# Kernel tuning notes

Hardware: AMD Instinct MI355X
Metric: run time of the kernel (lower is better)

The kernel has to match this reference:

```python
import jax, jax.numpy as jnp
import numpy as np

EPS = 1e-12
K_APPNP = 3
ALPHA = 0.5

def setup_inputs() -> dict:
    key = jax.random.key(0)
    kg, kz, k1, k2, k3 = jax.random.split(key, 5)
    N, out_dim, hid_dim = 10000, 128, 256
    g = jax.random.uniform(kg, (N, N), dtype=jnp.float32)
    z = jax.random.normal(kz, (N, out_dim), dtype=jnp.float32)
    def xavier(k, shape):
        fan_out, fan_in = shape
        lim = float(np.sqrt(6.0 / (fan_in + fan_out)))
        return jax.random.uniform(k, shape, jnp.float32, -lim, lim)
    # torch Linear weight is [out_features, in_features]
    W1 = xavier(k1, (hid_dim, out_dim))    # res1: out_dim -> hid_dim
    W1_ = xavier(k2, (hid_dim, hid_dim))   # res1_: hid -> hid
    W2 = xavier(k3, (out_dim, hid_dim))    # res2: hid -> out_dim
    return {"g": g, "z": z, "W1": W1, "W1_": W1_, "W2": W2}

def _graph_conv(g, x, W, act):
    # dropout is identity in eval mode
    return act((g @ x) @ W.T)

def _appnp(g, H):
    Z = H
    for _ in range(K_APPNP):
        Z = (1.0 - ALPHA) * (g @ Z) + ALPHA * H
    return Z

def reference(g, z, W1, W1_, W2):
    z1 = _graph_conv(g, z, W1, jax.nn.relu)       # [N, hid]
    z_ = _graph_conv(g, z1, W1_, jax.nn.relu)     # [N, hid]
    # torch.tensor(z_) detaches from the autograd graph
    zn = jax.lax.stop_gradient(z_)
    norm = jnp.maximum(jnp.linalg.norm(zn, axis=1, keepdims=True), EPS)
    zn = zn / norm                                 # F.normalize(p=2, dim=1)
    Z = _appnp(g, zn)                              # [N, hid]
    res = _graph_conv(g, z_, W2, jax.nn.sigmoid)   # [N, out]
    return (res, Z)
```

## Files before the change

kernel.cpp:

```cpp
#include <hip/hip_runtime.h>
#include <stdint.h>

typedef __attribute__((ext_vector_type(8))) short short8;
typedef __attribute__((ext_vector_type(4))) float f32x4;
typedef __attribute__((ext_vector_type(4))) unsigned short us4;

#define MFMA16(a,b,c) __builtin_amdgcn_mfma_f32_16x16x32_bf16((a),(b),(c),0,0,0)

static __device__ __forceinline__ float bf2f(unsigned short u){
  union { float f; unsigned int i; } c; c.i = ((unsigned int)u) << 16; return c.f;
}
static __device__ __forceinline__ unsigned short f2bf(float f){
  union { float f; unsigned int i; } c; c.f = f;
  unsigned int x = c.i;
  unsigned int r = x + 0x7fffu + ((x >> 16) & 1u);
  return (unsigned short)(r >> 16);
}

typedef const __attribute__((address_space(1))) void cg_void;
typedef __attribute__((address_space(3))) void lds_void;
static __device__ __forceinline__ void gl_lds16(const void* g, void* l){
  __builtin_amdgcn_global_load_lds((cg_void*)g, (lds_void*)l, 16, 0, 0);
}

#define MROWS 10240LL

__global__ void k_conv_g(const float* __restrict__ g, unsigned short* __restrict__ o){
  const int CH = 2512;
  const long long total = 10240LL * CH;
  for (long long i = (long long)blockIdx.x*blockDim.x + threadIdx.x; i < total;
       i += (long long)gridDim.x*blockDim.x){
    int r = (int)(i / CH);
    int c4 = (int)(i % CH) * 4;
    us4 v = {0,0,0,0};
    if (r < 10000 && c4 < 10000){
      float4 f = *(const float4*)(g + (long long)r*10000 + c4);
      v.x = f2bf(f.x); v.y = f2bf(f.y); v.z = f2bf(f.z); v.w = f2bf(f.w);
    }
    *(us4*)(o + (long long)r*10048 + c4) = v;
  }
}

__global__ void k_conv_w(const float* __restrict__ a, unsigned short* __restrict__ oa, int na4,
                         const float* __restrict__ b, unsigned short* __restrict__ ob, int nb4,
                         const float* __restrict__ c, unsigned short* __restrict__ oc, int nc4){
  for (int i = blockIdx.x*blockDim.x + threadIdx.x; i < na4 + nb4 + nc4;
       i += gridDim.x*blockDim.x){
    const float* src; unsigned short* dst; int j = i;
    if (j < na4){ src = a; dst = oa; }
    else if (j < na4 + nb4){ j -= na4; src = b; dst = ob; }
    else { j -= na4 + nb4; src = c; dst = oc; }
    float4 f = *(const float4*)(src + (long long)j*4);
    us4 v; v.x=f2bf(f.x); v.y=f2bf(f.y); v.z=f2bf(f.z); v.w=f2bf(f.w);
    *(us4*)(dst + (long long)j*4) = v;
  }
}

__global__ void k_tconv_z(const float* __restrict__ z, unsigned short* __restrict__ o){
  __shared__ unsigned short t[64][65];
  const int rb = blockIdx.x*64, cb = blockIdx.y*64;
  #pragma unroll
  for (int it = 0; it < 4; ++it){
    int idx = it*256 + threadIdx.x;
    int r = idx >> 4, c4 = (idx & 15) * 4;
    float4 f = {0.f,0.f,0.f,0.f};
    if (rb + r < 10000) f = *(const float4*)(z + (long long)(rb+r)*128 + cb + c4);
    t[c4+0][r] = f2bf(f.x); t[c4+1][r] = f2bf(f.y);
    t[c4+2][r] = f2bf(f.z); t[c4+3][r] = f2bf(f.w);
  }
  __syncthreads();
  #pragma unroll
  for (int it = 0; it < 4; ++it){
    int idx = it*256 + threadIdx.x;
    int ro = idx >> 4, co4 = (idx & 15) * 4;
    us4 v; v.x=t[ro][co4]; v.y=t[ro][co4+1]; v.z=t[ro][co4+2]; v.w=t[ro][co4+3];
    *(us4*)(o + (long long)(cb+ro)*10048 + rb + co4) = v;
  }
}

__global__ void k_t_bf16(const unsigned short* __restrict__ in, unsigned short* __restrict__ o){
  __shared__ unsigned short t[64][65];
  const int rb = blockIdx.x*64, cb = blockIdx.y*64;
  #pragma unroll
  for (int it = 0; it < 4; ++it){
    int idx = it*256 + threadIdx.x;
    int r = idx >> 4, c4 = (idx & 15) * 4;
    us4 v = {0,0,0,0};
    if (rb + r < 10000) v = *(const us4*)(in + (long long)(rb+r)*256 + cb + c4);
    t[c4+0][r]=v.x; t[c4+1][r]=v.y; t[c4+2][r]=v.z; t[c4+3][r]=v.w;
  }
  __syncthreads();
  #pragma unroll
  for (int it = 0; it < 4; ++it){
    int idx = it*256 + threadIdx.x;
    int ro = idx >> 4, co4 = (idx & 15)*4;
    us4 v; v.x=t[ro][co4]; v.y=t[ro][co4+1]; v.z=t[ro][co4+2]; v.w=t[ro][co4+3];
    *(us4*)(o + (long long)(cb+ro)*10048 + rb + co4) = v;
  }
}

__global__ __launch_bounds__(512)
void k_gemm8(const unsigned short* __restrict__ A,
             const unsigned short* __restrict__ B,
             float* __restrict__ P, int S, int ldp)
{
  constexpr int LDA = 10048;
  __shared__ unsigned short sm[2][32768];

  const int tid = threadIdx.x;
  const int wid = tid >> 6, l = tid & 63;
  const int wm = wid >> 2, wn = wid & 3;
  const int lr = l & 15, lk = l >> 4;
  const int mBase = blockIdx.x * 256;
  const int nBase = blockIdx.y * 256;
  const int s = blockIdx.z;
  const int kt0 = (157 * s) / S, kt1 = (157 * (s + 1)) / S;

  const unsigned short* gsrc[8];
  int ldst[8];
  #pragma unroll
  for (int h = 0; h < 4; ++h){
    const unsigned short* base = (h < 2) ? A : B;
    const int rowBase = ((h < 2) ? mBase : nBase) + (h & 1) * 128;
    const int ldsOff = ((h < 2) ? 0 : 16384) + (h & 1) * 8192;
    #pragma unroll
    for (int i = 0; i < 2; ++i){
      int ch = tid + 512 * i;
      int row = ch >> 3, gc = (ch & 7) ^ (row & 7);
      gsrc[h*2+i] = base + (long long)(rowBase + row) * LDA + gc * 8;
      ldst[h*2+i] = ldsOff + ch * 8;
    }
  }
  auto stage_tile = [&](unsigned short* dst, int kt){
    const long long ko = (long long)kt * 64;
    #pragma unroll
    for (int i = 0; i < 8; ++i)
      gl_lds16(gsrc[i] + ko, dst + ldst[i]);
  };

  f32x4 acc[8][4];
  #pragma unroll
  for (int i = 0; i < 8; ++i)
    #pragma unroll
    for (int j = 0; j < 4; ++j){ f32x4 zz = {0.f,0.f,0.f,0.f}; acc[i][j] = zz; }

  stage_tile(&sm[0][0], kt0);

  int cur = 0;
  for (int kt = kt0; kt < kt1; ++kt){
    const bool pf = (kt + 1 < kt1);
    unsigned short* nb = &sm[cur ^ 1][0];
    const unsigned short* sp = &sm[cur][0];

    if (pf){
      stage_tile(nb, kt + 1);
      __builtin_amdgcn_sched_barrier(0);
      asm volatile("s_waitcnt vmcnt(8)" ::: "memory");
    } else {
      asm volatile("s_waitcnt vmcnt(0)" ::: "memory");
    }
    __builtin_amdgcn_sched_barrier(0);
    __builtin_amdgcn_s_barrier();
    __builtin_amdgcn_sched_barrier(0);

    short8 bfr[4][2];
    #pragma unroll
    for (int jj = 0; jj < 4; ++jj){
      const int row = wn*64 + jj*16 + lr;
      #pragma unroll
      for (int ks = 0; ks < 2; ++ks)
        bfr[jj][ks] = *(const short8*)(sp + 16384 + row*64 + (((ks*4 + lk) ^ (row & 7)) * 8));
    }
    #pragma unroll
    for (int ih = 0; ih < 2; ++ih){
      short8 af[4][2];
      #pragma unroll
      for (int ii = 0; ii < 4; ++ii){
        const int row = wm*128 + ih*64 + ii*16 + lr;
        #pragma unroll
        for (int ks = 0; ks < 2; ++ks)
          af[ii][ks] = *(const short8*)(sp + row*64 + (((ks*4 + lk) ^ (row & 7)) * 8));
      }
      __builtin_amdgcn_s_setprio(1);
      #pragma unroll
      for (int ks = 0; ks < 2; ++ks)
        #pragma unroll
        for (int ii = 0; ii < 4; ++ii)
          #pragma unroll
          for (int jj = 0; jj < 4; ++jj)
            acc[ih*4+ii][jj] = MFMA16(af[ii][ks], bfr[jj][ks], acc[ih*4+ii][jj]);
      __builtin_amdgcn_s_setprio(0);
    }
    __builtin_amdgcn_sched_barrier(0);
    __builtin_amdgcn_s_barrier();
    __builtin_amdgcn_sched_barrier(0);
    cur ^= 1;
  }

  float* Pp = P + (long long)s * MROWS * ldp;
  #pragma unroll
  for (int i = 0; i < 8; ++i){
    const int row0 = mBase + wm*128 + i*16 + lk*4;
    #pragma unroll
    for (int j = 0; j < 4; ++j){
      const int col = nBase + wn*64 + j*16 + lr;
      #pragma unroll
      for (int r = 0; r < 4; ++r)
        Pp[(long long)(row0 + r)*ldp + col] = acc[i][j][r];
    }
  }
}

template<int BN, int NWM, int NWN>
__global__ __launch_bounds__(256)
void k_gemm(const unsigned short* __restrict__ A,
            const unsigned short* __restrict__ B,
            float* __restrict__ P, int S, int ldp)
{
  constexpr int LDA = 10048;
  constexpr int BM  = 64;
  constexpr int WM = BM / NWM, WN = BN / NWN;
  constexpr int MF = WM / 16, NF = WN / 16;
  constexpr int AE = BM * 64;
  constexpr int BE = BN * 64;
  constexpr int ACH = BM * 8 / 256;
  constexpr int BCH = BN * 8 / 256;

  __shared__ unsigned short sm[2][AE + BE];

  const int tid = threadIdx.x, w = tid >> 6, l = tid & 63;
  const int lr = l & 15, lk = l >> 4, swz = l & 7;
  const int wm = w / NWN, wn = w % NWN;
  const int mBase = blockIdx.x * BM;
  const int nBase = blockIdx.y * BN;
  const int s = blockIdx.z;
  const int kt0 = (157 * s) / S, kt1 = (157 * (s + 1)) / S;

  auto stage = [&](int buf, int kt){
    unsigned short* dst = &sm[buf][0];
    const unsigned short* Ak = A + (long long)kt * 64;
    const unsigned short* Bk = B + (long long)kt * 64;
    #pragma unroll
    for (int i = 0; i < ACH; ++i){
      int c = i * 256 + tid;
      int row = c >> 3, gr = c & 7;
      gl_lds16(Ak + (long long)(mBase + row) * LDA + ((gr ^ (row & 7)) * 8),
               dst + c * 8);
    }
    #pragma unroll
    for (int i = 0; i < BCH; ++i){
      int c = i * 256 + tid;
      int row = c >> 3, gr = c & 7;
      gl_lds16(Bk + (long long)(nBase + row) * LDA + ((gr ^ (row & 7)) * 8),
               dst + AE + c * 8);
    }
  };

  f32x4 acc[MF][NF];
  #pragma unroll
  for (int i = 0; i < MF; ++i)
    #pragma unroll
    for (int j = 0; j < NF; ++j){ f32x4 zz = {0.f,0.f,0.f,0.f}; acc[i][j] = zz; }

  stage(0, kt0);
  int cur = 0;
  for (int kt = kt0; kt < kt1; ++kt){
    __syncthreads();
    if (kt + 1 < kt1) stage(cur ^ 1, kt + 1);
    const unsigned short* sp = &sm[cur][0];
    #pragma unroll
    for (int ks = 0; ks < 2; ++ks){
      short8 a[MF], b[NF];
      #pragma unroll
      for (int i = 0; i < MF; ++i){
        int row = wm * WM + i * 16 + lr;
        a[i] = *(const short8*)(sp + row * 64 + (((4*ks + lk) ^ swz) * 8));
      }
      #pragma unroll
      for (int j = 0; j < NF; ++j){
        int row = wn * WN + j * 16 + lr;
        b[j] = *(const short8*)(sp + AE + row * 64 + (((4*ks + lk) ^ swz) * 8));
      }
      #pragma unroll
      for (int i = 0; i < MF; ++i)
        #pragma unroll
        for (int j = 0; j < NF; ++j)
          acc[i][j] = MFMA16(a[i], b[j], acc[i][j]);
    }
    cur ^= 1;
  }

  float* Pp = P + (long long)s * MROWS * ldp;
  #pragma unroll
  for (int i = 0; i < MF; ++i){
    const int row0 = mBase + wm * WM + i * 16 + lk * 4;
    #pragma unroll
    for (int j = 0; j < NF; ++j){
      const int col = nBase + wn * WN + j * 16 + lr;
      #pragma unroll
      for (int r = 0; r < 4; ++r)
        Pp[(long long)(row0 + r) * ldp + col] = acc[i][j][r];
    }
  }
}

template<int EPI>
__global__ void k_reduce(const float* __restrict__ P, int S, int ldp, int colOff,
                         int lg, void* __restrict__ out, int ldc,
                         const unsigned short* __restrict__ H)
{
  const long long stride = MROWS * ldp;
  const int idx = blockIdx.x * 256 + threadIdx.x;
  const int row = idx >> lg;
  const int c4 = (idx & ((1 << lg) - 1)) * 4;
  const float* p = P + (long long)row * ldp + colOff + c4;
  float4 sv = *(const float4*)p;
  for (int s2 = 1; s2 < S; ++s2){
    float4 t = *(const float4*)(p + (long long)s2 * stride);
    sv.x += t.x; sv.y += t.y; sv.z += t.z; sv.w += t.w;
  }
  if constexpr (EPI == 2){
    us4 h = *(const us4*)(H + (long long)row * 256 + c4);
    sv.x = 0.5f*sv.x + 0.5f*bf2f(h.x);
    sv.y = 0.5f*sv.y + 0.5f*bf2f(h.y);
    sv.z = 0.5f*sv.z + 0.5f*bf2f(h.z);
    sv.w = 0.5f*sv.w + 0.5f*bf2f(h.w);
    *(float4*)((float*)out + (long long)row * ldc + c4) = sv;
  } else {
    us4 o; o.x=f2bf(sv.x); o.y=f2bf(sv.y); o.z=f2bf(sv.z); o.w=f2bf(sv.w);
    *(us4*)((unsigned short*)out + (long long)row * ldc + c4) = o;
  }
}

__global__ void k_reduce_T(const float* __restrict__ P, int S, int ldp, int colOff,
                           unsigned short* __restrict__ outT,
                           const unsigned short* __restrict__ H)
{
  __shared__ unsigned short t[64][65];
  const int rb = blockIdx.x*64, cb = blockIdx.y*64;
  const long long stride = MROWS * (long long)ldp;
  #pragma unroll
  for (int it = 0; it < 4; ++it){
    int idx = it*256 + threadIdx.x;
    int r = idx >> 4, c4 = (idx & 15)*4;
    int row = rb + r;
    float4 sv = {0.f,0.f,0.f,0.f};
    if (row < 10000){
      const float* p = P + (long long)row*ldp + colOff + cb + c4;
      sv = *(const float4*)p;
      for (int s2 = 1; s2 < S; ++s2){
        float4 tt = *(const float4*)(p + (long long)s2*stride);
        sv.x += tt.x; sv.y += tt.y; sv.z += tt.z; sv.w += tt.w;
      }
      us4 h = *(const us4*)(H + (long long)row*256 + cb + c4);
      sv.x = 0.5f*sv.x + 0.5f*bf2f(h.x);
      sv.y = 0.5f*sv.y + 0.5f*bf2f(h.y);
      sv.z = 0.5f*sv.z + 0.5f*bf2f(h.z);
      sv.w = 0.5f*sv.w + 0.5f*bf2f(h.w);
    }
    t[c4+0][r] = f2bf(sv.x); t[c4+1][r] = f2bf(sv.y);
    t[c4+2][r] = f2bf(sv.z); t[c4+3][r] = f2bf(sv.w);
  }
  __syncthreads();
  #pragma unroll
  for (int it = 0; it < 4; ++it){
    int idx = it*256 + threadIdx.x;
    int ro = idx >> 4, co4 = (idx & 15)*4;
    us4 v; v.x=t[ro][co4]; v.y=t[ro][co4+1]; v.z=t[ro][co4+2]; v.w=t[ro][co4+3];
    *(us4*)(outT + (long long)(cb+ro)*10048 + rb + co4) = v;
  }
}

template<int NW, int KW, int ACT, int DONORM>
__global__ __launch_bounds__(320)
void k_gemm_small(const unsigned short* __restrict__ A,
                  const unsigned short* __restrict__ W,
                  void* __restrict__ out, unsigned short* __restrict__ out2)
{
  const int tid = threadIdx.x, w = tid >> 6, l = tid & 63;
  const int lr = l & 15, lk = l >> 4;
  const int mBase = blockIdx.x * 80;
  constexpr int NF = NW/16;

  f32x4 acc[NF];
  #pragma unroll
  for (int f = 0; f < NF; ++f){ f32x4 zz = {0.f,0.f,0.f,0.f}; acc[f] = zz; }

  const unsigned short* ap = A + (long long)(mBase + 16*w + lr)*KW + lk*8;
  #pragma unroll
  for (int kc = 0; kc < KW/32; ++kc){
    short8 a = *(const short8*)(ap + kc*32);
    #pragma unroll
    for (int f = 0; f < NF; ++f){
      short8 b = *(const short8*)(W + (long long)(16*f + lr)*KW + kc*32 + lk*8);
      acc[f] = MFMA16(a, b, acc[f]);
    }
  }

  const int row0 = mBase + 16*w + lk*4;
  if constexpr (DONORM){
    float ss[4] = {0.f,0.f,0.f,0.f};
    #pragma unroll
    for (int f = 0; f < NF; ++f)
      #pragma unroll
      for (int r = 0; r < 4; ++r){
        float v = fmaxf(acc[f][r], 0.0f);
        acc[f][r] = v;
        ss[r] += v*v;
      }
    #pragma unroll
    for (int r = 0; r < 4; ++r){
      #pragma unroll
      for (int off = 1; off <= 8; off <<= 1)
        ss[r] += __shfl_xor(ss[r], off, 64);
      ss[r] = 1.0f / fmaxf(sqrtf(ss[r]), 1e-12f);
    }
    #pragma unroll
    for (int f = 0; f < NF; ++f){
      const int col = 16*f + lr;
      #pragma unroll
      for (int r = 0; r < 4; ++r){
        const long long idx = (long long)(row0 + r)*NW + col;
        ((unsigned short*)out)[idx] = f2bf(acc[f][r]);
        out2[idx] = f2bf(acc[f][r] * ss[r]);
      }
    }
  } else {
    #pragma unroll
    for (int f = 0; f < NF; ++f){
      const int col = 16*f + lr;
      #pragma unroll
      for (int r = 0; r < 4; ++r){
        const long long idx = (long long)(row0 + r)*NW + col;
        float v = acc[f][r];
        if constexpr (ACT == 0) ((unsigned short*)out)[idx] = f2bf(fmaxf(v, 0.0f));
        else                    ((float*)out)[idx] = 1.0f / (1.0f + expf(-v));
      }
    }
  }
}

extern "C" void kernel_launch(void* const* d_in, const int* in_sizes, int n_in,
                              void* d_out, int out_size, void* d_ws, size_t ws_size,
                              hipStream_t stream)
{
  const float* g   = (const float*)d_in[0];
  const float* z   = (const float*)d_in[1];
  const float* W1  = (const float*)d_in[2];
  const float* W1_ = (const float*)d_in[3];
  const float* W2  = (const float*)d_in[4];

  char* ws = (char*)d_ws;
  size_t off = 0;
  auto alloc = [&](size_t bytes)->void*{
    void* p = ws + off; off += (bytes + 255) & ~(size_t)255; return p;
  };
  unsigned short* g16  = (unsigned short*)alloc(10240ULL*10048*2);
  unsigned short* zT   = (unsigned short*)alloc(128ULL*10048*2);
  unsigned short* W1c  = (unsigned short*)alloc(256ULL*128*2);
  unsigned short* W1_c = (unsigned short*)alloc(256ULL*256*2);
  unsigned short* W2c  = (unsigned short*)alloc(128ULL*256*2);
  unsigned short* tbuf = (unsigned short*)alloc(10000ULL*256*2);
  unsigned short* Xbuf = (unsigned short*)alloc(10000ULL*256*2);
  unsigned short* Tbuf = (unsigned short*)alloc(512ULL*10048*2);
  unsigned short* zn   = (unsigned short*)alloc(10000ULL*256*2);
  float*          P    = (float*)alloc(10240ULL*1536*4);
  (void)ws_size; (void)in_sizes; (void)n_in; (void)out_size;

  float* res  = (float*)d_out;
  float* Zout = (float*)d_out + 10000LL*128;

  k_conv_g<<<dim3(2048), dim3(256), 0, stream>>>(g, g16);
  k_tconv_z<<<dim3(157,2), dim3(256), 0, stream>>>(z, zT);
  k_conv_w<<<dim3(120), dim3(256), 0, stream>>>(W1, W1c, 256*128/4,
                                                W1_, W1_c, 256*256/4,
                                                W2, W2c, 128*256/4);

  k_gemm<128,2,2><<<dim3(157,1,3), dim3(256), 0, stream>>>(g16, zT, P, 3, 128);
  k_reduce<0><<<dim3(1250), dim3(256), 0, stream>>>(P, 3, 128, 0, 5, tbuf, 128, nullptr);
  k_gemm_small<256,128,0,0><<<dim3(125), dim3(320), 0, stream>>>(tbuf, W1c, Xbuf, nullptr);
  k_t_bf16<<<dim3(157,4), dim3(256), 0, stream>>>(Xbuf, Tbuf);
  k_gemm8<<<dim3(40,1,6), dim3(512), 0, stream>>>(g16, Tbuf, P, 6, 256);
  k_reduce<0><<<dim3(2500), dim3(256), 0, stream>>>(P, 6, 256, 0, 6, tbuf, 256, nullptr);
  k_gemm_small<256,256,0,1><<<dim3(125), dim3(320), 0, stream>>>(tbuf, W1_c, Xbuf, zn);
  k_t_bf16<<<dim3(157,4), dim3(256), 0, stream>>>(Xbuf, Tbuf);
  k_t_bf16<<<dim3(157,4), dim3(256), 0, stream>>>(zn, Tbuf + 256LL*10048);
  k_gemm8<<<dim3(40,2,3), dim3(512), 0, stream>>>(g16, Tbuf, P, 3, 512);
  k_reduce<0><<<dim3(2500), dim3(256), 0, stream>>>(P, 3, 512, 0, 6, tbuf, 256, nullptr);
  k_reduce_T<<<dim3(157,4), dim3(256), 0, stream>>>(P, 3, 512, 256, Tbuf, zn);
  k_gemm_small<128,256,1,0><<<dim3(125), dim3(320), 0, stream>>>(tbuf, W2c, res, nullptr);
  k_gemm8<<<dim3(40,1,6), dim3(512), 0, stream>>>(g16, Tbuf, P, 6, 256);
  k_reduce_T<<<dim3(157,4), dim3(256), 0, stream>>>(P, 6, 256, 0, Tbuf, zn);
  k_gemm8<<<dim3(40,1,6), dim3(512), 0, stream>>>(g16, Tbuf, P, 6, 256);
  k_reduce<2><<<dim3(2500), dim3(256), 0, stream>>>(P, 6, 256, 0, 6, Zout, 256, zn);
}
```

Measured before the change: 643.4 us.

## Fuse g bf16 conversion into first GEMM, fold reductions into small GEMMs, bf16 partials

The first propagation GEMM now reads fp32 g directly, converts it to bf16 in registers, and writes the bf16 copy for later GEMMs. This removes the separate full conversion pass over the 10000x10000 matrix. Split-K partial outputs are stored as bf16 instead of fp32, which halves partial traffic but adds rounding error to every partial sum. The separate reduce and transpose kernels are folded into small-GEMM kernels that sum the partials and write transposed output directly, with a zero-fill kernel for the padding regions.

```diff
diff --git a/kernel.cpp b/kernel.cpp
--- a/kernel.cpp
+++ b/kernel.cpp
@@ -16,6 +16,12 @@
   unsigned int r = x + 0x7fffu + ((x >> 16) & 1u);
   return (unsigned short)(r >> 16);
 }
+static __device__ __forceinline__ short8 pack8(const float* v){
+  short8 r;
+  #pragma unroll
+  for (int i = 0; i < 8; ++i) r[i] = (short)f2bf(v[i]);
+  return r;
+}
 
 typedef const __attribute__((address_space(1))) void cg_void;
 typedef __attribute__((address_space(3))) void lds_void;
@@ -24,20 +30,17 @@
 }
 
 #define MROWS 10240LL
-
-__global__ void k_conv_g(const float* __restrict__ g, unsigned short* __restrict__ o){
-  const int CH = 2512;
-  const long long total = 10240LL * CH;
-  for (long long i = (long long)blockIdx.x*blockDim.x + threadIdx.x; i < total;
-       i += (long long)gridDim.x*blockDim.x){
-    int r = (int)(i / CH);
-    int c4 = (int)(i % CH) * 4;
-    us4 v = {0,0,0,0};
-    if (r < 10000 && c4 < 10000){
-      float4 f = *(const float4*)(g + (long long)r*10000 + c4);
-      v.x = f2bf(f.x); v.y = f2bf(f.y); v.z = f2bf(f.z); v.w = f2bf(f.w);
-    }
-    *(us4*)(o + (long long)r*10048 + c4) = v;
+#define LDA   10048
+
+__global__ void k_zero(unsigned short* __restrict__ g16, unsigned short* __restrict__ Tbuf){
+  const long long i0 = (long long)blockIdx.x*256 + threadIdx.x;
+  const long long NG = 192LL*LDA/8;
+  short8 z = {0,0,0,0,0,0,0,0};
+  for (long long c = i0; c < NG; c += (long long)gridDim.x*256)
+    *(short8*)(g16 + 10048LL*LDA + c*8) = z;
+  for (long long c = i0; c < 512*6; c += (long long)gridDim.x*256){
+    int row = (int)(c/6), k = (int)(c%6);
+    *(short8*)(Tbuf + (long long)row*LDA + 10000 + k*8) = z;
   }
 }
 
@@ -74,37 +77,121 @@
     int idx = it*256 + threadIdx.x;
     int ro = idx >> 4, co4 = (idx & 15) * 4;
     us4 v; v.x=t[ro][co4]; v.y=t[ro][co4+1]; v.z=t[ro][co4+2]; v.w=t[ro][co4+3];
-    *(us4*)(o + (long long)(cb+ro)*10048 + rb + co4) = v;
-  }
-}
-
-__global__ void k_t_bf16(const unsigned short* __restrict__ in, unsigned short* __restrict__ o){
-  __shared__ unsigned short t[64][65];
-  const int rb = blockIdx.x*64, cb = blockIdx.y*64;
-  #pragma unroll
-  for (int it = 0; it < 4; ++it){
-    int idx = it*256 + threadIdx.x;
-    int r = idx >> 4, c4 = (idx & 15) * 4;
-    us4 v = {0,0,0,0};
-    if (rb + r < 10000) v = *(const us4*)(in + (long long)(rb+r)*256 + cb + c4);
-    t[c4+0][r]=v.x; t[c4+1][r]=v.y; t[c4+2][r]=v.z; t[c4+3][r]=v.w;
-  }
-  __syncthreads();
-  #pragma unroll
-  for (int it = 0; it < 4; ++it){
-    int idx = it*256 + threadIdx.x;
-    int ro = idx >> 4, co4 = (idx & 15)*4;
-    us4 v; v.x=t[ro][co4]; v.y=t[ro][co4+1]; v.z=t[ro][co4+2]; v.w=t[ro][co4+3];
-    *(us4*)(o + (long long)(cb+ro)*10048 + rb + co4) = v;
+    *(us4*)(o + (long long)(cb+ro)*LDA + rb + co4) = v;
+  }
+}
+
+__global__ __launch_bounds__(256)
+void k_gemm_t0(const float* __restrict__ g, const unsigned short* __restrict__ zT,
+               unsigned short* __restrict__ g16, unsigned short* __restrict__ P, int S)
+{
+  constexpr int ldp = 128;
+  __shared__ unsigned short sm[2][(64+128)*64];
+  const int tid = threadIdx.x, w = tid >> 6, l = tid & 63;
+  const int lr = l & 15, lk = l >> 4;
+  const int wm = w >> 1, wn = w & 1;
+  const int mBase = blockIdx.x * 64;
+  const int s = blockIdx.z;
+  const int kt0 = (157*s)/S, kt1 = (157*(s+1))/S;
+
+  int arow[2], acol8[2];
+  #pragma unroll
+  for (int i = 0; i < 2; ++i){
+    int ch = tid + 256*i;
+    int row = ch >> 3, gr = ch & 7;
+    arow[i] = row; acol8[i] = (gr ^ (row & 7)) * 8;
+  }
+  float fA[2][8];
+  auto loadA = [&](int kt){
+    #pragma unroll
+    for (int i = 0; i < 2; ++i){
+      int grow = mBase + arow[i];
+      int col = kt*64 + acol8[i];
+      if (grow < 10000 && col < 10000){
+        float4 x = *(const float4*)(g + (long long)grow*10000 + col);
+        float4 y = *(const float4*)(g + (long long)grow*10000 + col + 4);
+        fA[i][0]=x.x; fA[i][1]=x.y; fA[i][2]=x.z; fA[i][3]=x.w;
+        fA[i][4]=y.x; fA[i][5]=y.y; fA[i][6]=y.z; fA[i][7]=y.w;
+      } else {
+        #pragma unroll
+        for (int j = 0; j < 8; ++j) fA[i][j] = 0.f;
+      }
+    }
+  };
+  auto writeA = [&](int buf, int kt){
+    #pragma unroll
+    for (int i = 0; i < 2; ++i){
+      int ch = tid + 256*i;
+      short8 v = pack8(fA[i]);
+      *(short8*)(&sm[buf][ch*8]) = v;
+      *(short8*)(g16 + (long long)(mBase + arow[i])*LDA + kt*64 + acol8[i]) = v;
+    }
+  };
+  auto stageB = [&](int buf, int kt){
+    unsigned short* dst = &sm[buf][64*64];
+    const unsigned short* Bk = zT + (long long)kt*64;
+    #pragma unroll
+    for (int i = 0; i < 4; ++i){
+      int c = i*256 + tid; int row = c >> 3, gr = c & 7;
+      gl_lds16(Bk + (long long)row*LDA + ((gr ^ (row & 7))*8), dst + c*8);
+    }
+  };
+
+  f32x4 acc[2][4];
+  #pragma unroll
+  for (int i = 0; i < 2; ++i)
+    #pragma unroll
+    for (int j = 0; j < 4; ++j){ f32x4 zz = {0.f,0.f,0.f,0.f}; acc[i][j] = zz; }
+
+  loadA(kt0); stageB(0, kt0); writeA(0, kt0);
+  int cur = 0;
+  for (int kt = kt0; kt < kt1; ++kt){
+    __syncthreads();
+    const bool pf = (kt + 1 < kt1);
+    if (pf){ loadA(kt+1); stageB(cur^1, kt+1); }
+    const unsigned short* sp = &sm[cur][0];
+    #pragma unroll
+    for (int ks = 0; ks < 2; ++ks){
+      short8 a[2], b[4];
+      #pragma unroll
+      for (int i = 0; i < 2; ++i){
+        int row = wm*32 + i*16 + lr;
+        a[i] = *(const short8*)(sp + row*64 + (((4*ks+lk) ^ (row & 7))*8));
+      }
+      #pragma unroll
+      for (int j = 0; j < 4; ++j){
+        int rb = wn*64 + j*16 + lr;
+        b[j] = *(const short8*)(sp + 64*64 + rb*64 + (((4*ks+lk) ^ (rb & 7))*8));
+      }
+      #pragma unroll
+      for (int i = 0; i < 2; ++i)
+        #pragma unroll
+        for (int j = 0; j < 4; ++j)
+          acc[i][j] = MFMA16(a[i], b[j], acc[i][j]);
+    }
+    if (pf) writeA(cur^1, kt+1);
+    cur ^= 1;
+  }
+
+  unsigned short* Pp = P + (long long)s*MROWS*ldp;
+  #pragma unroll
+  for (int i = 0; i < 2; ++i){
+    const int row0 = mBase + wm*32 + i*16 + lk*4;
+    #pragma unroll
+    for (int j = 0; j < 4; ++j){
+      const int col = wn*64 + j*16 + lr;
+      #pragma unroll
+      for (int r = 0; r < 4; ++r)
+        Pp[(long long)(row0+r)*ldp + col] = f2bf(acc[i][j][r]);
+    }
   }
 }
 
 __global__ __launch_bounds__(512)
 void k_gemm8(const unsigned short* __restrict__ A,
              const unsigned short* __restrict__ B,
-             float* __restrict__ P, int S, int ldp)
-{
-  constexpr int LDA = 10048;
+             unsigned short* __restrict__ P, int S, int ldp)
+{
   __shared__ unsigned short sm[2][32768];
 
   const int tid = threadIdx.x;
@@ -114,7 +201,7 @@
   const int mBase = blockIdx.x * 256;
   const int nBase = blockIdx.y * 256;
   const int s = blockIdx.z;
-  const int kt0 = (157 * s) / S, kt1 = (157 * (s + 1)) / S;
+  const int kt0 = (157*s)/S, kt1 = (157*(s+1))/S;
 
   const unsigned short* gsrc[8];
   int ldst[8];
@@ -125,10 +212,10 @@
     const int ldsOff = ((h < 2) ? 0 : 16384) + (h & 1) * 8192;
     #pragma unroll
     for (int i = 0; i < 2; ++i){
-      int ch = tid + 512 * i;
+      int ch = tid + 512*i;
       int row = ch >> 3, gc = (ch & 7) ^ (row & 7);
-      gsrc[h*2+i] = base + (long long)(rowBase + row) * LDA + gc * 8;
-      ldst[h*2+i] = ldsOff + ch * 8;
+      gsrc[h*2+i] = base + (long long)(rowBase + row)*LDA + gc*8;
+      ldst[h*2+i] = ldsOff + ch*8;
     }
   }
   auto stage_tile = [&](unsigned short* dst, int kt){
@@ -169,7 +256,7 @@
       const int row = wn*64 + jj*16 + lr;
       #pragma unroll
       for (int ks = 0; ks < 2; ++ks)
-        bfr[jj][ks] = *(const short8*)(sp + 16384 + row*64 + (((ks*4 + lk) ^ (row & 7)) * 8));
+        bfr[jj][ks] = *(const short8*)(sp + 16384 + row*64 + (((ks*4+lk) ^ (row & 7))*8));
     }
     #pragma unroll
     for (int ih = 0; ih < 2; ++ih){
@@ -179,7 +266,7 @@
         const int row = wm*128 + ih*64 + ii*16 + lr;
         #pragma unroll
         for (int ks = 0; ks < 2; ++ks)
-          af[ii][ks] = *(const short8*)(sp + row*64 + (((ks*4 + lk) ^ (row & 7)) * 8));
+          af[ii][ks] = *(const short8*)(sp + row*64 + (((ks*4+lk) ^ (row & 7))*8));
       }
       __builtin_amdgcn_s_setprio(1);
       #pragma unroll
@@ -197,7 +284,7 @@
     cur ^= 1;
   }
 
-  float* Pp = P + (long long)s * MROWS * ldp;
+  unsigned short* Pp = P + (long long)s*MROWS*ldp;
   #pragma unroll
   for (int i = 0; i < 8; ++i){
     const int row0 = mBase + wm*128 + i*16 + lk*4;
@@ -206,133 +293,102 @@
       const int col = nBase + wn*64 + j*16 + lr;
       #pragma unroll
       for (int r = 0; r < 4; ++r)
-        Pp[(long long)(row0 + r)*ldp + col] = acc[i][j][r];
-    }
-  }
-}
-
-template<int BN, int NWM, int NWN>
-__global__ __launch_bounds__(256)
-void k_gemm(const unsigned short* __restrict__ A,
-            const unsigned short* __restrict__ B,
-            float* __restrict__ P, int S, int ldp)
-{
-  constexpr int LDA = 10048;
-  constexpr int BM  = 64;
-  constexpr int WM = BM / NWM, WN = BN / NWN;
-  constexpr int MF = WM / 16, NF = WN / 16;
-  constexpr int AE = BM * 64;
-  constexpr int BE = BN * 64;
-  constexpr int ACH = BM * 8 / 256;
-  constexpr int BCH = BN * 8 / 256;
-
-  __shared__ unsigned short sm[2][AE + BE];
-
+        Pp[(long long)(row0+r)*ldp + col] = f2bf(acc[i][j][r]);
+    }
+  }
+}
+
+template<int NW, int KW, int LDP, int S, int MODE>
+__global__ __launch_bounds__(320)
+void k_small(const unsigned short* __restrict__ P,
+             const unsigned short* __restrict__ W,
+             unsigned short* __restrict__ o1,
+             unsigned short* __restrict__ o2,
+             unsigned short* __restrict__ o3,
+             float* __restrict__ of)
+{
   const int tid = threadIdx.x, w = tid >> 6, l = tid & 63;
-  const int lr = l & 15, lk = l >> 4, swz = l & 7;
-  const int wm = w / NWN, wn = w % NWN;
-  const int mBase = blockIdx.x * BM;
-  const int nBase = blockIdx.y * BN;
-  const int s = blockIdx.z;
-  const int kt0 = (157 * s) / S, kt1 = (157 * (s + 1)) / S;
-
-  auto stage = [&](int buf, int kt){
-    unsigned short* dst = &sm[buf][0];
-    const unsigned short* Ak = A + (long long)kt * 64;
-    const unsigned short* Bk = B + (long long)kt * 64;
-    #pragma unroll
-    for (int i = 0; i < ACH; ++i){
-      int c = i * 256 + tid;
-      int row = c >> 3, gr = c & 7;
-      gl_lds16(Ak + (long long)(mBase + row) * LDA + ((gr ^ (row & 7)) * 8),
-               dst + c * 8);
-    }
-    #pragma unroll
-    for (int i = 0; i < BCH; ++i){
-      int c = i * 256 + tid;
-      int row = c >> 3, gr = c & 7;
-      gl_lds16(Bk + (long long)(nBase + row) * LDA + ((gr ^ (row & 7)) * 8),
-               dst + AE + c * 8);
-    }
-  };
-
-  f32x4 acc[MF][NF];
-  #pragma unroll
-  for (int i = 0; i < MF; ++i)
-    #pragma unroll
-    for (int j = 0; j < NF; ++j){ f32x4 zz = {0.f,0.f,0.f,0.f}; acc[i][j] = zz; }
-
-  stage(0, kt0);
-  int cur = 0;
-  for (int kt = kt0; kt < kt1; ++kt){
-    __syncthreads();
-    if (kt + 1 < kt1) stage(cur ^ 1, kt + 1);
-    const unsigned short* sp = &sm[cur][0];
-    #pragma unroll
-    for (int ks = 0; ks < 2; ++ks){
-      short8 a[MF], b[NF];
-      #pragma unroll
-      for (int i = 0; i < MF; ++i){
-        int row = wm * WM + i * 16 + lr;
-        a[i] = *(const short8*)(sp + row * 64 + (((4*ks + lk) ^ swz) * 8));
-      }
-      #pragma unroll
-      for (int j = 0; j < NF; ++j){
-        int row = wn * WN + j * 16 + lr;
-        b[j] = *(const short8*)(sp + AE + row * 64 + (((4*ks + lk) ^ swz) * 8));
-      }
-      #pragma unroll
-      for (int i = 0; i < MF; ++i)
-        #pragma unroll
-        for (int j = 0; j < NF; ++j)
-          acc[i][j] = MFMA16(a[i], b[j], acc[i][j]);
-    }
-    cur ^= 1;
-  }
-
-  float* Pp = P + (long long)s * MROWS * ldp;
-  #pragma unroll
-  for (int i = 0; i < MF; ++i){
-    const int row0 = mBase + wm * WM + i * 16 + lk * 4;
-    #pragma unroll
-    for (int j = 0; j < NF; ++j){
-      const int col = nBase + wn * WN + j * 16 + lr;
+  const int lr = l & 15, lk = l >> 4;
+  const int mBase = blockIdx.x * 80;
+  constexpr int NF = NW/16;
+  constexpr long long SSTR = MROWS*(long long)LDP;
+
+  f32x4 acc[NF];
+  #pragma unroll
+  for (int f = 0; f < NF; ++f){ f32x4 zz = {0.f,0.f,0.f,0.f}; acc[f] = zz; }
+
+  const unsigned short* ap = P + (long long)(mBase + 16*w + lr)*LDP + lk*8;
+  #pragma unroll
+  for (int kc = 0; kc < KW/32; ++kc){
+    float av[8];
+    short8 v0 = *(const short8*)(ap + kc*32);
+    #pragma unroll
+    for (int e = 0; e < 8; ++e) av[e] = bf2f((unsigned short)v0[e]);
+    #pragma unroll
+    for (int s2 = 1; s2 < S; ++s2){
+      short8 v = *(const short8*)(ap + (long long)s2*SSTR + kc*32);
+      #pragma unroll
+      for (int e = 0; e < 8; ++e) av[e] += bf2f((unsigned short)v[e]);
+    }
+    short8 a = pack8(av);
+    #pragma unroll
+    for (int f = 0; f < NF; ++f){
+      short8 b = *(const short8*)(W + (long long)(16*f+lr)*KW + kc*32 + lk*8);
+      acc[f] = MFMA16(a, b, acc[f]);
+    }
+  }
+
+  const int row0 = mBase + 16*w + lk*4;
+  if constexpr (MODE == 2){
+    #pragma unroll
+    for (int f = 0; f < NF; ++f){
+      const int col = 16*f + lr;
       #pragma unroll
       for (int r = 0; r < 4; ++r)
-        Pp[(long long)(row0 + r) * ldp + col] = acc[i][j][r];
-    }
-  }
-}
-
-template<int EPI>
-__global__ void k_reduce(const float* __restrict__ P, int S, int ldp, int colOff,
-                         int lg, void* __restrict__ out, int ldc,
-                         const unsigned short* __restrict__ H)
-{
-  const long long stride = MROWS * ldp;
-  const int idx = blockIdx.x * 256 + threadIdx.x;
-  const int row = idx >> lg;
-  const int c4 = (idx & ((1 << lg) - 1)) * 4;
-  const float* p = P + (long long)row * ldp + colOff + c4;
-  float4 sv = *(const float4*)p;
-  for (int s2 = 1; s2 < S; ++s2){
-    float4 t = *(const float4*)(p + (long long)s2 * stride);
-    sv.x += t.x; sv.y += t.y; sv.z += t.z; sv.w += t.w;
-  }
-  if constexpr (EPI == 2){
-    us4 h = *(const us4*)(H + (long long)row * 256 + c4);
-    sv.x = 0.5f*sv.x + 0.5f*bf2f(h.x);
-    sv.y = 0.5f*sv.y + 0.5f*bf2f(h.y);
-    sv.z = 0.5f*sv.z + 0.5f*bf2f(h.z);
-    sv.w = 0.5f*sv.w + 0.5f*bf2f(h.w);
-    *(float4*)((float*)out + (long long)row * ldc + c4) = sv;
+        of[(long long)(row0+r)*NW + col] = 1.0f / (1.0f + expf(-acc[f][r]));
+    }
+  } else if constexpr (MODE == 0){
+    #pragma unroll
+    for (int f = 0; f < NF; ++f){
+      us4 v;
+      #pragma unroll
+      for (int r = 0; r < 4; ++r) v[r] = f2bf(fmaxf(acc[f][r], 0.0f));
+      *(us4*)(o1 + (long long)(16*f+lr)*LDA + row0) = v;
+    }
   } else {
-    us4 o; o.x=f2bf(sv.x); o.y=f2bf(sv.y); o.z=f2bf(sv.z); o.w=f2bf(sv.w);
-    *(us4*)((unsigned short*)out + (long long)row * ldc + c4) = o;
-  }
-}
-
-__global__ void k_reduce_T(const float* __restrict__ P, int S, int ldp, int colOff,
+    float ss[4] = {0.f,0.f,0.f,0.f};
+    #pragma unroll
+    for (int f = 0; f < NF; ++f)
+      #pragma unroll
+      for (int r = 0; r < 4; ++r){
+        float v = fmaxf(acc[f][r], 0.0f);
+        acc[f][r] = v;
+        ss[r] += v*v;
+      }
+    #pragma unroll
+    for (int r = 0; r < 4; ++r){
+      #pragma unroll
+      for (int off = 1; off <= 8; off <<= 1)
+        ss[r] += __shfl_xor(ss[r], off, 64);
+      ss[r] = 1.0f / fmaxf(sqrtf(ss[r]), 1e-12f);
+    }
+    #pragma unroll
+    for (int f = 0; f < NF; ++f){
+      const int col = 16*f + lr;
+      us4 vz, vn;
+      #pragma unroll
+      for (int r = 0; r < 4; ++r){
+        vz[r] = f2bf(acc[f][r]);
+        vn[r] = f2bf(acc[f][r]*ss[r]);
+        o3[(long long)(row0+r)*256 + col] = vn[r];
+      }
+      *(us4*)(o1 + (long long)col*LDA + row0) = vz;
+      *(us4*)(o2 + (long long)col*LDA + row0) = vn;
+    }
+  }
+}
+
+__global__ void k_reduce_T(const unsigned short* __restrict__ P, int S, int ldp, int colOff,
                            unsigned short* __restrict__ outT,
                            const unsigned short* __restrict__ H)
 {
@@ -344,22 +400,22 @@
     int idx = it*256 + threadIdx.x;
     int r = idx >> 4, c4 = (idx & 15)*4;
     int row = rb + r;
-    float4 sv = {0.f,0.f,0.f,0.f};
+    float sv[4] = {0.f,0.f,0.f,0.f};
     if (row < 10000){
-      const float* p = P + (long long)row*ldp + colOff + cb + c4;
-      sv = *(const float4*)p;
-      for (int s2 = 1; s2 < S; ++s2){
-        float4 tt = *(const float4*)(p + (long long)s2*stride);
-        sv.x += tt.x; sv.y += tt.y; sv.z += tt.z; sv.w += tt.w;
+      const unsigned short* p = P + (long long)row*ldp + colOff + cb + c4;
+      for (int s2 = 0; s2 < S; ++s2){
+        us4 tt = *(const us4*)(p + (long long)s2*stride);
+        sv[0] += bf2f(tt.x); sv[1] += bf2f(tt.y);
+        sv[2] += bf2f(tt.z); sv[3] += bf2f(tt.w);
       }
       us4 h = *(const us4*)(H + (long long)row*256 + cb + c4);
-      sv.x = 0.5f*sv.x + 0.5f*bf2f(h.x);
-      sv.y = 0.5f*sv.y + 0.5f*bf2f(h.y);
-      sv.z = 0.5f*sv.z + 0.5f*bf2f(h.z);
-      sv.w = 0.5f*sv.w + 0.5f*bf2f(h.w);
-    }
-    t[c4+0][r] = f2bf(sv.x); t[c4+1][r] = f2bf(sv.y);
-    t[c4+2][r] = f2bf(sv.z); t[c4+3][r] = f2bf(sv.w);
+      sv[0] = 0.5f*sv[0] + 0.5f*bf2f(h.x);
+      sv[1] = 0.5f*sv[1] + 0.5f*bf2f(h.y);
+      sv[2] = 0.5f*sv[2] + 0.5f*bf2f(h.z);
+      sv[3] = 0.5f*sv[3] + 0.5f*bf2f(h.w);
+    }
+    t[c4+0][r] = f2bf(sv[0]); t[c4+1][r] = f2bf(sv[1]);
+    t[c4+2][r] = f2bf(sv[2]); t[c4+3][r] = f2bf(sv[3]);
   }
   __syncthreads();
   #pragma unroll
@@ -367,77 +423,31 @@
     int idx = it*256 + threadIdx.x;
     int ro = idx >> 4, co4 = (idx & 15)*4;
     us4 v; v.x=t[ro][co4]; v.y=t[ro][co4+1]; v.z=t[ro][co4+2]; v.w=t[ro][co4+3];
-    *(us4*)(outT + (long long)(cb+ro)*10048 + rb + co4) = v;
-  }
-}
-
-template<int NW, int KW, int ACT, int DONORM>
-__global__ __launch_bounds__(320)
-void k_gemm_small(const unsigned short* __restrict__ A,
-                  const unsigned short* __restrict__ W,
-                  void* __restrict__ out, unsigned short* __restrict__ out2)
-{
-  const int tid = threadIdx.x, w = tid >> 6, l = tid & 63;
-  const int lr = l & 15, lk = l >> 4;
-  const int mBase = blockIdx.x * 80;
-  constexpr int NF = NW/16;
-
-  f32x4 acc[NF];
-  #pragma unroll
-  for (int f = 0; f < NF; ++f){ f32x4 zz = {0.f,0.f,0.f,0.f}; acc[f] = zz; }
-
-  const unsigned short* ap = A + (long long)(mBase + 16*w + lr)*KW + lk*8;
-  #pragma unroll
-  for (int kc = 0; kc < KW/32; ++kc){
-    short8 a = *(const short8*)(ap + kc*32);
-    #pragma unroll
-    for (int f = 0; f < NF; ++f){
-      short8 b = *(const short8*)(W + (long long)(16*f + lr)*KW + kc*32 + lk*8);
-      acc[f] = MFMA16(a, b, acc[f]);
-    }
-  }
-
-  const int row0 = mBase + 16*w + lk*4;
-  if constexpr (DONORM){
-    float ss[4] = {0.f,0.f,0.f,0.f};
-    #pragma unroll
-    for (int f = 0; f < NF; ++f)
-      #pragma unroll
-      for (int r = 0; r < 4; ++r){
-        float v = fmaxf(acc[f][r], 0.0f);
-        acc[f][r] = v;
-        ss[r] += v*v;
-      }
-    #pragma unroll
-    for (int r = 0; r < 4; ++r){
-      #pragma unroll
-      for (int off = 1; off <= 8; off <<= 1)
-        ss[r] += __shfl_xor(ss[r], off, 64);
-      ss[r] = 1.0f / fmaxf(sqrtf(ss[r]), 1e-12f);
-    }
-    #pragma unroll
-    for (int f = 0; f < NF; ++f){
-      const int col = 16*f + lr;
-      #pragma unroll
-      for (int r = 0; r < 4; ++r){
-        const long long idx = (long long)(row0 + r)*NW + col;
-        ((unsigned short*)out)[idx] = f2bf(acc[f][r]);
-        out2[idx] = f2bf(acc[f][r] * ss[r]);
-      }
-    }
-  } else {
-    #pragma unroll
-    for (int f = 0; f < NF; ++f){
-      const int col = 16*f + lr;
-      #pragma unroll
-      for (int r = 0; r < 4; ++r){
-        const long long idx = (long long)(row0 + r)*NW + col;
-        float v = acc[f][r];
-        if constexpr (ACT == 0) ((unsigned short*)out)[idx] = f2bf(fmaxf(v, 0.0f));
-        else                    ((float*)out)[idx] = 1.0f / (1.0f + expf(-v));
-      }
-    }
-  }
+    *(us4*)(outT + (long long)(cb+ro)*LDA + rb + co4) = v;
+  }
+}
+
+__global__ void k_reduce2(const unsigned short* __restrict__ P, int S, int ldp,
+                          float* __restrict__ out, const unsigned short* __restrict__ H)
+{
+  const long long stride = MROWS * (long long)ldp;
+  const int idx = blockIdx.x*256 + threadIdx.x;
+  const int row = idx >> 6;
+  const int c4 = (idx & 63)*4;
+  const unsigned short* p = P + (long long)row*ldp + c4;
+  float sv[4] = {0.f,0.f,0.f,0.f};
+  for (int s2 = 0; s2 < S; ++s2){
+    us4 tt = *(const us4*)(p + (long long)s2*stride);
+    sv[0] += bf2f(tt.x); sv[1] += bf2f(tt.y);
+    sv[2] += bf2f(tt.z); sv[3] += bf2f(tt.w);
+  }
+  us4 h = *(const us4*)(H + (long long)row*256 + c4);
+  float4 o;
+  o.x = 0.5f*sv[0] + 0.5f*bf2f(h.x);
+  o.y = 0.5f*sv[1] + 0.5f*bf2f(h.y);
+  o.z = 0.5f*sv[2] + 0.5f*bf2f(h.z);
+  o.w = 0.5f*sv[3] + 0.5f*bf2f(h.w);
+  *(float4*)(out + (long long)row*256 + c4) = o;
 }
 
 extern "C" void kernel_launch(void* const* d_in, const int* in_sizes, int n_in,
@@ -460,37 +470,30 @@
   unsigned short* W1c  = (unsigned short*)alloc(256ULL*128*2);
   unsigned short* W1_c = (unsigned short*)alloc(256ULL*256*2);
   unsigned short* W2c  = (unsigned short*)alloc(128ULL*256*2);
-  unsigned short* tbuf = (unsigned short*)alloc(10000ULL*256*2);
-  unsigned short* Xbuf = (unsigned short*)alloc(10000ULL*256*2);
   unsigned short* Tbuf = (unsigned short*)alloc(512ULL*10048*2);
   unsigned short* zn   = (unsigned short*)alloc(10000ULL*256*2);
-  float*          P    = (float*)alloc(10240ULL*1536*4);
+  unsigned short* P    = (unsigned short*)alloc(10240ULL*1536*2);
   (void)ws_size; (void)in_sizes; (void)n_in; (void)out_size;
 
   float* res  = (float*)d_out;
   float* Zout = (float*)d_out + 10000LL*128;
-
-  k_conv_g<<<dim3(2048), dim3(256), 0, stream>>>(g, g16);
+  unsigned short* znT = Tbuf + 256LL*10048;
+
+  k_zero<<<dim3(512), dim3(256), 0, stream>>>(g16, Tbuf);
   k_tconv_z<<<dim3(157,2), dim3(256), 0, stream>>>(z, zT);
   k_conv_w<<<dim3(120), dim3(256), 0, stream>>>(W1, W1c, 256*128/4,
                                                 W1_, W1_c, 256*256/4,
                                                 W2, W2c, 128*256/4);
 
-  k_gemm<128,2,2><<<dim3(157,1,3), dim3(256), 0, stream>>>(g16, zT, P, 3, 128);
-  k_reduce<0><<<dim3(1250), dim3(256), 0, stream>>>(P, 3, 128, 0, 5, tbuf, 128, nullptr);
-  k_gemm_small<256,128,0,0><<<dim3(125), dim3(320), 0, stream>>>(tbuf, W1c, Xbuf, nullptr);
-  k_t_bf16<<<dim3(157,4), dim3(256), 0, stream>>>(Xbuf, Tbuf);
+  k_gemm_t0<<<dim3(157,1,3), dim3(256), 0, stream>>>(g, zT, g16, P, 3);
+  k_small<256,128,128,3,0><<<dim3(125), dim3(320), 0, stream>>>(P, W1c, Tbuf, nullptr, nullptr, nullptr);
   k_gemm8<<<dim3(40,1,6), dim3(512), 0, stream>>>(g16, Tbuf, P, 6, 256);
-  k_reduce<0><<<dim3(2500), dim3(256), 0, stream>>>(P, 6, 256, 0, 6, tbuf, 256, nullptr);
-  k_gemm_small<256,256,0,1><<<dim3(125), dim3(320), 0, stream>>>(tbuf, W1_c, Xbuf, zn);
-  k_t_bf16<<<dim3(157,4), dim3(256), 0, stream>>>(Xbuf, Tbuf);
-  k_t_bf16<<<dim3(157,4), dim3(256), 0, stream>>>(zn, Tbuf + 256LL*10048);
+  k_small<256,256,256,6,1><<<dim3(125), dim3(320), 0, stream>>>(P, W1_c, Tbuf, znT, zn, nullptr);
   k_gemm8<<<dim3(40,2,3), dim3(512), 0, stream>>>(g16, Tbuf, P, 3, 512);
-  k_reduce<0><<<dim3(2500), dim3(256), 0, stream>>>(P, 3, 512, 0, 6, tbuf, 256, nullptr);
+  k_small<128,256,512,3,2><<<dim3(125), dim3(320), 0, stream>>>(P, W2c, nullptr, nullptr, nullptr, res);
   k_reduce_T<<<dim3(157,4), dim3(256), 0, stream>>>(P, 3, 512, 256, Tbuf, zn);
-  k_gemm_small<128,256,1,0><<<dim3(125), dim3(320), 0, stream>>>(tbuf, W2c, res, nullptr);
   k_gemm8<<<dim3(40,1,6), dim3(512), 0, stream>>>(g16, Tbuf, P, 6, 256);
   k_reduce_T<<<dim3(157,4), dim3(256), 0, stream>>>(P, 6, 256, 0, Tbuf, zn);
   k_gemm8<<<dim3(40,1,6), dim3(512), 0, stream>>>(g16, Tbuf, P, 6, 256);
-  k_reduce<2><<<dim3(2500), dim3(256), 0, stream>>>(P, 6, 256, 0, 6, Zout, 256, zn);
-}
+  k_reduce2<<<dim3(2500), dim3(256), 0, stream>>>(P, 6, 256, Zout, zn);
+}
```

After: 558.7 us. 13.2% less time.
